# Optimization experiments

Measured on AMD Instinct MI355X. Metric: run time of the kernel, lower is better.

Reference implementation:

```python
import jax, jax.numpy as jnp
import numpy as np

B, L, D, H = 2, 2048, 2048, 16
DH = D // H

def setup_inputs() -> dict:
    key = jax.random.key(0)
    ks = jax.random.split(key, 7)
    q = jax.random.normal(ks[0], (B, L, D), dtype=jnp.float32)
    k = jax.random.normal(ks[1], (B, L, D), dtype=jnp.float32)
    v = jax.random.normal(ks[2], (B, L, D), dtype=jnp.float32)
    # causal mask: True means masked (matches torch masked_fill semantics)
    attn_mask = jnp.triu(jnp.ones((L, L), dtype=bool), k=1)[None, None, :, :]
    scale = 0.02
    wq = jax.random.normal(ks[3], (D, D), dtype=jnp.float32) * scale
    wk = jax.random.normal(ks[4], (D, D), dtype=jnp.float32) * scale
    wv = jax.random.normal(ks[5], (D, D), dtype=jnp.float32) * scale
    wo = jax.random.normal(ks[6], (D, D), dtype=jnp.float32) * scale
    return {"q": q, "k": k, "v": v, "attn_mask": attn_mask,
            "wq": wq, "wk": wk, "wv": wv, "wo": wo}

def _split_heads(x):
    b, l, _ = x.shape
    return x.reshape(b, l, H, DH).transpose(0, 2, 1, 3)  # [B,H,L,DH]

def reference(q, k, v, attn_mask, wq, wk, wv, wo):
    # torch Linear: y = x @ W.T (bias=False)
    qh = _split_heads(q @ wq.T)
    kh = _split_heads(k @ wk.T)
    vh = _split_heads(v @ wv.T)
    scale = 1.0 / np.sqrt(DH).astype(np.float32)
    scores = jnp.einsum('bhqd,bhkd->bhqk', qh, kh) * scale
    neg = jnp.finfo(scores.dtype).min
    scores = jnp.where(attn_mask, neg, scores)
    attn = jax.nn.softmax(scores, axis=-1)
    ctx = jnp.einsum('bhqk,bhkd->bhqd', attn, vh)
    ctx = ctx.transpose(0, 2, 1, 3).reshape(q.shape[0], q.shape[1], D)
    return ctx @ wo.T
```

## Files before the change

kernel.cpp:

```cpp
#include <hip/hip_runtime.h>

#define B_  2
#define L_  2048
#define D_  2048
#define H_  16
#define DH_ 128
#define K_  2048
#define M_  4096

typedef __attribute__((ext_vector_type(8))) short bf16x8;
typedef __attribute__((ext_vector_type(4))) float f32x4;
typedef __attribute__((ext_vector_type(4))) float float4v;
typedef __attribute__((ext_vector_type(8))) unsigned short u16x8;

__device__ __forceinline__ unsigned short f2bf(float f) {
  unsigned u = __builtin_bit_cast(unsigned, f);
  u += 0x7fffu + ((u >> 16) & 1u);
  return (unsigned short)(u >> 16);
}

typedef __attribute__((address_space(3))) unsigned int lds_uint;
typedef __attribute__((address_space(1))) const unsigned int glob_uint;
__device__ __forceinline__ void gld16(const void* g, void* l) {
  __builtin_amdgcn_global_load_lds((glob_uint*)g, (lds_uint*)l, 16, 0, 0);
}

__global__ void cvt_all(const float* __restrict__ wq, const float* __restrict__ wk,
                        const float* __restrict__ wv, const float* __restrict__ wo,
                        const float* __restrict__ q, const float* __restrict__ k,
                        const float* __restrict__ v, unsigned short* __restrict__ ws,
                        int nacts) {
  const size_t DD = (size_t)D_ * D_;
  const size_t BLD = (size_t)B_ * L_ * D_;
  const int z = blockIdx.z;
  const float* src;
  unsigned short* dst;
  size_t nelem;
  if (z < 4) {
    src = (z == 0) ? wq : (z == 1) ? wk : (z == 2) ? wv : wo;
    dst = ws + (size_t)z * DD;
    nelem = DD;
  } else {
    if (z - 4 >= nacts) return;
    src = (z == 4) ? q : (z == 5) ? k : v;
    dst = ws + 4 * DD + (size_t)(z - 4) * BLD;
    nelem = BLD;
  }
  size_t i = ((size_t)blockIdx.x * 256 + threadIdx.x) * 8;
  if (i >= nelem) return;
  float4v x0 = *(const float4v*)(src + i);
  float4v x1 = *(const float4v*)(src + i + 4);
  u16x8 p;
  p[0]=f2bf(x0[0]); p[1]=f2bf(x0[1]); p[2]=f2bf(x0[2]); p[3]=f2bf(x0[3]);
  p[4]=f2bf(x1[0]); p[5]=f2bf(x1[1]); p[6]=f2bf(x1[2]); p[7]=f2bf(x1[3]);
  *(u16x8*)(dst + i) = p;
}

template <bool ABF16>
__global__ __launch_bounds__(256, 2) void proj_gemm(
    const void* __restrict__ a0, const void* __restrict__ a1, const void* __restrict__ a2,
    const unsigned short* __restrict__ wqb, const unsigned short* __restrict__ wkb,
    const unsigned short* __restrict__ wvb,
    unsigned short* __restrict__ Qh, unsigned short* __restrict__ Kh,
    unsigned short* __restrict__ Vt) {
  __shared__ unsigned short smem[128 * 136];
  unsigned short* As = smem;
  unsigned short* Bs = smem + 128 * 64;

  const int z = blockIdx.z;
  const void* A = (z == 0) ? a0 : (z == 1) ? a1 : a2;
  const unsigned short* W = (z == 0) ? wqb : (z == 1) ? wkb : wvb;

  const int tid = threadIdx.x;
  const int wave = tid >> 6, lane = tid & 63;
  const int wr = wave >> 1, wc = wave & 1;
  const int bm0 = blockIdx.x * 128;
  const int bn0 = blockIdx.y * 128;
  const int l15 = lane & 15, l4 = lane >> 4;

  f32x4 acc[4][4];
#pragma unroll
  for (int m = 0; m < 4; m++)
#pragma unroll
    for (int n = 0; n < 4; n++) { f32x4 zz = {0.f, 0.f, 0.f, 0.f}; acc[m][n] = zz; }

  for (int k0 = 0; k0 < K_; k0 += 64) {
#pragma unroll
    for (int it = 0; it < 4; ++it) {
      const int base = it * 256 + wave * 64;
      const int ch = base + lane;
      const int r = ch >> 3, c = ch & 7;
      gld16(W + (size_t)(bn0 + r) * K_ + (k0 + c * 8), Bs + base * 8);
    }
    if (ABF16) {
#pragma unroll
      for (int it = 0; it < 4; ++it) {
        const int base = it * 256 + wave * 64;
        const int ch = base + lane;
        const int r = ch >> 3, c = ch & 7;
        gld16((const unsigned short*)A + (size_t)(bm0 + r) * K_ + (k0 + c * 8), As + base * 8);
      }
    } else {
#pragma unroll
      for (int it = 0; it < 4; ++it) {
        const int ch = it * 256 + tid;
        const int r = ch >> 3, c = ch & 7;
        const float* g = (const float*)A + (size_t)(bm0 + r) * K_ + (k0 + c * 8);
        float4v x0 = *(const float4v*)g;
        float4v x1 = *(const float4v*)(g + 4);
        u16x8 p;
        p[0]=f2bf(x0[0]); p[1]=f2bf(x0[1]); p[2]=f2bf(x0[2]); p[3]=f2bf(x0[3]);
        p[4]=f2bf(x1[0]); p[5]=f2bf(x1[1]); p[6]=f2bf(x1[2]); p[7]=f2bf(x1[3]);
        *(u16x8*)&As[ch * 8] = p;
      }
    }
    __syncthreads();
#pragma unroll
    for (int ks = 0; ks < 2; ++ks) {
      const int kc = ks * 32 + l4 * 8;
      bf16x8 af[4], bfr[4];
#pragma unroll
      for (int m = 0; m < 4; m++) af[m] = *(const bf16x8*)&As[(wr * 64 + m * 16 + l15) * 64 + kc];
#pragma unroll
      for (int n = 0; n < 4; n++) bfr[n] = *(const bf16x8*)&Bs[(wc * 64 + n * 16 + l15) * 64 + kc];
#pragma unroll
      for (int m = 0; m < 4; m++)
#pragma unroll
        for (int n = 0; n < 4; n++)
          acc[m][n] = __builtin_amdgcn_mfma_f32_16x16x32_bf16(af[m], bfr[n], acc[m][n], 0, 0, 0);
    }
    __syncthreads();
  }

  if (z < 2) {
    unsigned short* O = (z == 0) ? Qh : Kh;
#pragma unroll
    for (int m = 0; m < 4; m++) {
      const int rr = bm0 + wr * 64 + m * 16 + l4 * 4;
#pragma unroll
      for (int n = 0; n < 4; n++) {
        const int cc = bn0 + wc * 64 + n * 16 + l15;
        const int h = cc >> 7, dh = cc & 127;
#pragma unroll
        for (int j = 0; j < 4; j++) {
          const int r2 = rr + j;
          const int b = r2 >> 11, lr = r2 & 2047;
          O[((size_t)(b * H_ + h) * L_ + lr) * DH_ + dh] = f2bf(acc[m][n][j]);
        }
      }
    }
  } else {
    __syncthreads();
    unsigned short* T = smem;
#pragma unroll
    for (int m = 0; m < 4; m++)
#pragma unroll
      for (int n = 0; n < 4; n++) {
        const int cl = wc * 64 + n * 16 + l15;
        const int rl = wr * 64 + m * 16 + l4 * 4;
#pragma unroll
        for (int j = 0; j < 4; j++) T[cl * 136 + rl + j] = f2bf(acc[m][n][j]);
      }
    __syncthreads();
    const int b = bm0 >> 11, lbase = bm0 & 2047;
    const int hb = bn0 >> 7;
#pragma unroll
    for (int it = 0; it < 8; ++it) {
      const int idx = it * 256 + tid;
      const int dhl = idx >> 4, c = idx & 15;
      u16x8 val = *(const u16x8*)&T[dhl * 136 + c * 8];
      *(u16x8*)&Vt[((size_t)(b * H_ + hb) * DH_ + dhl) * L_ + lbase + c * 8] = val;
    }
  }
}

#define SCALE_ 0.08838834764831845f

__global__ __launch_bounds__(256, 2) void attn_kernel(
    const unsigned short* __restrict__ Qh, const unsigned short* __restrict__ Kh,
    const unsigned short* __restrict__ Vt, unsigned short* __restrict__ ctx) {
  __shared__ unsigned short Ks[128 * 128];
  __shared__ unsigned short Vs[128 * 128];
  __shared__ unsigned short Ps[4][16 * 128];

  const int pair = blockIdx.x, bh = blockIdx.y;
  const size_t hoff = (size_t)bh * L_ * DH_;
  const unsigned short* Qp = Qh + hoff;
  const unsigned short* Kp = Kh + hoff;
  const unsigned short* Vp = Vt + hoff;

  const int tid = threadIdx.x, wave = tid >> 6, lane = tid & 63;
  const int l15 = lane & 15, l4 = lane >> 4;
  const int b = bh >> 4, h = bh & 15;

#pragma unroll 1
  for (int p = 0; p < 2; ++p) {
    const int qt = p ? (31 - pair) : pair;
    const int ntiles = (qt + 2) >> 1;

    bf16x8 qf[4];
    {
      const int qrow = qt * 64 + wave * 16 + l15;
#pragma unroll
      for (int s = 0; s < 4; s++)
        qf[s] = *(const bf16x8*)&Qp[(size_t)qrow * DH_ + s * 32 + l4 * 8];
    }

    f32x4 o[8];
#pragma unroll
    for (int df = 0; df < 8; df++) { f32x4 zz = {0.f, 0.f, 0.f, 0.f}; o[df] = zz; }
    float m_r[4] = {-1e30f, -1e30f, -1e30f, -1e30f};
    float l_r[4] = {0.f, 0.f, 0.f, 0.f};

    for (int kt = 0; kt < ntiles; ++kt) {
#pragma unroll
      for (int it = 0; it < 8; ++it) {
        const int base = it * 256 + wave * 64;
        const int ch = base + lane;
        const int r = ch >> 4, s = ch & 15;
        gld16(Kp + (size_t)(kt * 128 + r) * DH_ + ((s ^ (r & 7)) * 8), (unsigned short*)Ks + base * 8);
      }
#pragma unroll
      for (int it = 0; it < 8; ++it) {
        const int base = it * 256 + wave * 64;
        const int ch = base + lane;
        const int r = ch >> 4, s = ch & 15;
        gld16(Vp + (size_t)r * L_ + kt * 128 + ((s ^ (r & 7)) * 8), (unsigned short*)Vs + base * 8);
      }
      __syncthreads();

      f32x4 sa[8];
#pragma unroll
      for (int f = 0; f < 8; f++) { f32x4 zz = {0.f, 0.f, 0.f, 0.f}; sa[f] = zz; }
#pragma unroll
      for (int ks = 0; ks < 4; ++ks) {
        const int c = ks * 4 + l4;
#pragma unroll
        for (int f = 0; f < 8; ++f) {
          const int n = f * 16 + l15;
          bf16x8 kf = *(const bf16x8*)&Ks[n * 128 + ((c ^ (n & 7)) * 8)];
          sa[f] = __builtin_amdgcn_mfma_f32_16x16x32_bf16(qf[ks], kf, sa[f], 0, 0, 0);
        }
      }

      const bool last = (kt == ntiles - 1);
#pragma unroll
      for (int f = 0; f < 8; f++) {
        const int kg = kt * 128 + f * 16 + l15;
#pragma unroll
        for (int j = 0; j < 4; j++) {
          float t = sa[f][j] * SCALE_;
          if (last && kg > qt * 64 + wave * 16 + l4 * 4 + j) t = -1e30f;
          sa[f][j] = t;
        }
      }

#pragma unroll
      for (int j = 0; j < 4; j++) {
        float mx = fmaxf(fmaxf(fmaxf(sa[0][j], sa[1][j]), fmaxf(sa[2][j], sa[3][j])),
                         fmaxf(fmaxf(sa[4][j], sa[5][j]), fmaxf(sa[6][j], sa[7][j])));
#pragma unroll
        for (int d = 1; d < 16; d <<= 1) mx = fmaxf(mx, __shfl_xor(mx, d));
        const float mnew = fmaxf(m_r[j], mx);
        const float alpha = __expf(m_r[j] - mnew);
        float rs = 0.f;
        const int row = l4 * 4 + j;
#pragma unroll
        for (int f = 0; f < 8; f++) {
          float pp = __expf(sa[f][j] - mnew);
          rs += pp;
          const int col = f * 16 + l15;
          const int c = col >> 3;
          Ps[wave][row * 128 + ((c ^ (row & 7)) * 8) + (col & 7)] = f2bf(pp);
        }
#pragma unroll
        for (int d = 1; d < 16; d <<= 1) rs += __shfl_xor(rs, d);
        l_r[j] = l_r[j] * alpha + rs;
        m_r[j] = mnew;
#pragma unroll
        for (int df = 0; df < 8; df++) o[df][j] *= alpha;
      }

#pragma unroll
      for (int ksl = 0; ksl < 4; ++ksl) {
        const int pc = ksl * 4 + l4;
        bf16x8 pf = *(const bf16x8*)&Ps[wave][l15 * 128 + ((pc ^ (l15 & 7)) * 8)];
#pragma unroll
        for (int df = 0; df < 8; ++df) {
          const int vr = df * 16 + l15;
          bf16x8 vf = *(const bf16x8*)&Vs[vr * 128 + ((pc ^ (vr & 7)) * 8)];
          o[df] = __builtin_amdgcn_mfma_f32_16x16x32_bf16(pf, vf, o[df], 0, 0, 0);
        }
      }
      __syncthreads();
    }

#pragma unroll
    for (int j = 0; j < 4; j++) {
      const float inv = 1.0f / l_r[j];
      const int lq = qt * 64 + wave * 16 + l4 * 4 + j;
      const size_t rowb = ((size_t)(b * L_ + lq)) * D_ + h * DH_;
#pragma unroll
      for (int df = 0; df < 8; ++df)
        ctx[rowb + df * 16 + l15] = f2bf(o[df][j] * inv);
    }
  }
}

__global__ __launch_bounds__(256, 2) void out_gemm(const unsigned short* __restrict__ ctx,
                                                   const unsigned short* __restrict__ wob,
                                                   float* __restrict__ out) {
  __shared__ unsigned short smem[2 * 128 * 64];
  unsigned short* As = smem;
  unsigned short* Bs = smem + 128 * 64;

  const int tid = threadIdx.x;
  const int wave = tid >> 6, lane = tid & 63;
  const int wr = wave >> 1, wc = wave & 1;
  const int bm0 = blockIdx.x * 128;
  const int bn0 = blockIdx.y * 128;
  const int l15 = lane & 15, l4 = lane >> 4;

  f32x4 acc[4][4];
#pragma unroll
  for (int m = 0; m < 4; m++)
#pragma unroll
    for (int n = 0; n < 4; n++) { f32x4 zz = {0.f, 0.f, 0.f, 0.f}; acc[m][n] = zz; }

  for (int k0 = 0; k0 < K_; k0 += 64) {
#pragma unroll
    for (int it = 0; it < 4; ++it) {
      const int base = it * 256 + wave * 64;
      const int ch = base + lane;
      const int r = ch >> 3, c = ch & 7;
      gld16(ctx + (size_t)(bm0 + r) * K_ + (k0 + c * 8), As + base * 8);
      gld16(wob + (size_t)(bn0 + r) * K_ + (k0 + c * 8), Bs + base * 8);
    }
    __syncthreads();
#pragma unroll
    for (int ks = 0; ks < 2; ++ks) {
      const int kc = ks * 32 + l4 * 8;
      bf16x8 af[4], bfr[4];
#pragma unroll
      for (int m = 0; m < 4; m++) af[m] = *(const bf16x8*)&As[(wr * 64 + m * 16 + l15) * 64 + kc];
#pragma unroll
      for (int n = 0; n < 4; n++) bfr[n] = *(const bf16x8*)&Bs[(wc * 64 + n * 16 + l15) * 64 + kc];
#pragma unroll
      for (int m = 0; m < 4; m++)
#pragma unroll
        for (int n = 0; n < 4; n++)
          acc[m][n] = __builtin_amdgcn_mfma_f32_16x16x32_bf16(af[m], bfr[n], acc[m][n], 0, 0, 0);
    }
    __syncthreads();
  }

#pragma unroll
  for (int m = 0; m < 4; m++) {
    const int rr = bm0 + wr * 64 + m * 16 + l4 * 4;
#pragma unroll
    for (int n = 0; n < 4; n++) {
      const int cc = bn0 + wc * 64 + n * 16 + l15;
#pragma unroll
      for (int j = 0; j < 4; j++) out[(size_t)(rr + j) * D_ + cc] = acc[m][n][j];
    }
  }
}

extern "C" void kernel_launch(void* const* d_in, const int* in_sizes, int n_in,
                              void* d_out, int out_size, void* d_ws, size_t ws_size,
                              hipStream_t stream) {
  const float* q  = (const float*)d_in[0];
  const float* k  = (const float*)d_in[1];
  const float* v  = (const float*)d_in[2];
  const float* wq = (const float*)d_in[4];
  const float* wk = (const float*)d_in[5];
  const float* wv = (const float*)d_in[6];
  const float* wo = (const float*)d_in[7];

  const size_t DD = (size_t)D_ * D_;
  const size_t BLD = (size_t)B_ * L_ * D_;
  unsigned short* ws  = (unsigned short*)d_ws;
  unsigned short* wqb = ws;
  unsigned short* wkb = wqb + DD;
  unsigned short* wvb = wkb + DD;
  unsigned short* wob = wvb + DD;

  const size_t need_full = (4 * DD + 7 * BLD) * 2;

  if (ws_size >= need_full) {
    unsigned short* qb  = wob + DD;
    unsigned short* kb  = qb + BLD;
    unsigned short* vb  = kb + BLD;
    unsigned short* QhP = vb + BLD;
    unsigned short* KhP = QhP + BLD;
    unsigned short* VtP = KhP + BLD;
    unsigned short* ctx = VtP + BLD;

    cvt_all<<<dim3(4096, 1, 7), 256, 0, stream>>>(wq, wk, wv, wo, q, k, v, ws, 3);
    proj_gemm<true><<<dim3(32, 16, 3), 256, 0, stream>>>(qb, kb, vb, wqb, wkb, wvb, QhP, KhP, VtP);
    attn_kernel<<<dim3(16, 32), 256, 0, stream>>>(QhP, KhP, VtP, ctx);
    out_gemm<<<dim3(32, 16), 256, 0, stream>>>(ctx, wob, (float*)d_out);
  } else {
    unsigned short* QhP = wob + DD;
    unsigned short* KhP = QhP + BLD;
    unsigned short* VtP = KhP + BLD;
    unsigned short* ctx = VtP + BLD;

    cvt_all<<<dim3(4096, 1, 4), 256, 0, stream>>>(wq, wk, wv, wo, q, k, v, ws, 0);
    proj_gemm<false><<<dim3(32, 16, 3), 256, 0, stream>>>(q, k, v, wqb, wkb, wvb, QhP, KhP, VtP);
    attn_kernel<<<dim3(16, 32), 256, 0, stream>>>(QhP, KhP, VtP, ctx);
    out_gemm<<<dim3(32, 16), 256, 0, stream>>>(ctx, wob, (float*)d_out);
  }
}
```

Measured before the change: 303.8 us.

## Replace projection and output GEMMs with triple-buffered 8-wave 128x256 GEMM

Adds a new gemm8 kernel with 512 threads and 128x256 tiles. It uses a three-stage LDS ring fed by direct global-to-LDS loads, XOR-swizzled LDS layouts, explicit vmcnt waits and barriers, s_setprio around MFMA bursts, and a block-index remap for L2 locality. It replaces both the QKV projection and the output projection, which previously used a single-buffered 128x128 GEMM that stalled on loads each k-step. The V transpose epilogue now uses vectorized swizzled LDS writes, and the attention kernel gets setprio hints around its MFMA loops. Costs are more LDS per block, which may lower occupancy, and more intricate synchronization.

```diff
diff --git a/kernel.cpp b/kernel.cpp
--- a/kernel.cpp
+++ b/kernel.cpp
@@ -6,12 +6,12 @@
 #define H_  16
 #define DH_ 128
 #define K_  2048
-#define M_  4096
 
 typedef __attribute__((ext_vector_type(8))) short bf16x8;
 typedef __attribute__((ext_vector_type(4))) float f32x4;
 typedef __attribute__((ext_vector_type(4))) float float4v;
 typedef __attribute__((ext_vector_type(8))) unsigned short u16x8;
+typedef __attribute__((ext_vector_type(4))) unsigned short u16x4;
 
 __device__ __forceinline__ unsigned short f2bf(float f) {
   unsigned u = __builtin_bit_cast(unsigned, f);
@@ -24,6 +24,9 @@
 __device__ __forceinline__ void gld16(const void* g, void* l) {
   __builtin_amdgcn_global_load_lds((glob_uint*)g, (lds_uint*)l, 16, 0, 0);
 }
+
+#define BAR() do { asm volatile("" ::: "memory"); __builtin_amdgcn_s_barrier(); asm volatile("" ::: "memory"); } while (0)
+#define VMCNT(n) asm volatile("s_waitcnt vmcnt(" #n ")" ::: "memory")
 
 __global__ void cvt_all(const float* __restrict__ wq, const float* __restrict__ wk,
                         const float* __restrict__ wv, const float* __restrict__ wo,
@@ -56,9 +59,192 @@
   *(u16x8*)(dst + i) = p;
 }
 
-template <bool ABF16>
-__global__ __launch_bounds__(256, 2) void proj_gemm(
-    const void* __restrict__ a0, const void* __restrict__ a1, const void* __restrict__ a2,
+template <int KIND>
+__global__ __launch_bounds__(512, 2) void gemm8(
+    const unsigned short* __restrict__ a0, const unsigned short* __restrict__ a1,
+    const unsigned short* __restrict__ a2,
+    const unsigned short* __restrict__ w0, const unsigned short* __restrict__ w1,
+    const unsigned short* __restrict__ w2,
+    unsigned short* __restrict__ Qh, unsigned short* __restrict__ Kh,
+    unsigned short* __restrict__ Vt, float* __restrict__ OF) {
+  __shared__ unsigned short smem[3 * 24576];
+
+  const int lin = blockIdx.x + 32 * (blockIdx.y + 8 * blockIdx.z);
+  const int cpx = KIND ? 32 : 96;
+  const int s = (lin & 7) * cpx + (lin >> 3);
+  const int mt = s & 31;
+  const int r_ = s >> 5;
+  const int ntile = KIND ? r_ : (r_ & 7);
+  const int z = KIND ? 0 : (r_ >> 3);
+
+  const unsigned short* A = KIND ? a0 : (z == 0 ? a0 : z == 1 ? a1 : a2);
+  const unsigned short* W = KIND ? w0 : (z == 0 ? w0 : z == 1 ? w1 : w2);
+  const int mode = KIND ? 2 : (z == 2 ? 1 : 0);
+
+  const int bm0 = mt * 128;
+  const int bn0 = ntile * 256;
+
+  const int tid = threadIdx.x;
+  const int wid = tid >> 6, lane = tid & 63;
+  const int wr = wid >> 2, wc = wid & 3;
+  const int l15 = lane & 15, l4 = lane >> 4;
+
+  const unsigned short* gsrc[6];
+  int ldst[6];
+  {
+#pragma unroll
+    for (int i = 0; i < 2; ++i) {
+      const int c = i * 512 + tid, r = c >> 3, s0 = c & 7;
+      gsrc[i] = A + (size_t)(bm0 + r) * K_ + ((s0 ^ (r & 7)) << 3);
+      ldst[i] = c * 8;
+    }
+#pragma unroll
+    for (int u = 0; u < 2; ++u)
+#pragma unroll
+      for (int i = 0; i < 2; ++i) {
+        const int c = i * 512 + tid, r = c >> 3, s0 = c & 7;
+        gsrc[2 + u * 2 + i] = W + (size_t)(bn0 + u * 128 + r) * K_ + ((s0 ^ (r & 7)) << 3);
+        ldst[2 + u * 2 + i] = 8192 + (u * 1024 + c) * 8;
+      }
+  }
+#define STAGE(idx, p) do { gld16(gsrc[idx], &smem[(p) * 24576 + ldst[idx]]); gsrc[idx] += 64; } while (0)
+
+  int offA[2][2][2], offB[4][2];
+#pragma unroll
+  for (int mh = 0; mh < 2; ++mh)
+#pragma unroll
+    for (int ml = 0; ml < 2; ++ml)
+#pragma unroll
+      for (int ks = 0; ks < 2; ++ks) {
+        const int row = wr * 64 + mh * 32 + ml * 16 + l15;
+        const int ch = ks * 4 + l4;
+        offA[mh][ml][ks] = row * 64 + ((ch ^ (row & 7)) << 3);
+      }
+#pragma unroll
+  for (int nf = 0; nf < 4; ++nf)
+#pragma unroll
+    for (int ks = 0; ks < 2; ++ks) {
+      const int rowb = wc * 64 + nf * 16 + l15;
+      const int ch = ks * 4 + l4;
+      offB[nf][ks] = 8192 + rowb * 64 + ((ch ^ (rowb & 7)) << 3);
+    }
+
+  f32x4 acc[4][4];
+#pragma unroll
+  for (int m = 0; m < 4; ++m)
+#pragma unroll
+    for (int n = 0; n < 4; ++n) { f32x4 zz = {0.f, 0.f, 0.f, 0.f}; acc[m][n] = zz; }
+
+  STAGE(0, 0); STAGE(1, 0); STAGE(2, 0); STAGE(3, 0); STAGE(4, 0); STAGE(5, 0);
+  STAGE(0, 1); STAGE(1, 1); STAGE(2, 1); STAGE(3, 1); STAGE(4, 1); STAGE(5, 1);
+  VMCNT(6);
+  BAR();
+
+  int p = 0;
+  for (int t = 0; t < 32; ++t) {
+    int p2 = p + 2; if (p2 >= 3) p2 -= 3;
+    const unsigned short* bA = &smem[p * 24576];
+    bf16x8 af[2][2], bfr[4][2];
+#pragma unroll
+    for (int ml = 0; ml < 2; ++ml)
+#pragma unroll
+      for (int ks = 0; ks < 2; ++ks)
+        af[ml][ks] = *(const bf16x8*)&bA[offA[0][ml][ks]];
+#pragma unroll
+    for (int nf = 0; nf < 4; ++nf)
+#pragma unroll
+      for (int ks = 0; ks < 2; ++ks)
+        bfr[nf][ks] = *(const bf16x8*)&bA[offB[nf][ks]];
+    if (t < 30) { STAGE(0, p2); STAGE(1, p2); STAGE(2, p2); STAGE(3, p2); }
+    BAR();
+    __builtin_amdgcn_s_setprio(1);
+#pragma unroll
+    for (int ml = 0; ml < 2; ++ml)
+#pragma unroll
+      for (int nf = 0; nf < 4; ++nf)
+#pragma unroll
+        for (int ks = 0; ks < 2; ++ks)
+          acc[ml][nf] = __builtin_amdgcn_mfma_f32_16x16x32_bf16(af[ml][ks], bfr[nf][ks], acc[ml][nf], 0, 0, 0);
+    __builtin_amdgcn_s_setprio(0);
+    BAR();
+#pragma unroll
+    for (int ml = 0; ml < 2; ++ml)
+#pragma unroll
+      for (int ks = 0; ks < 2; ++ks)
+        af[ml][ks] = *(const bf16x8*)&bA[offA[1][ml][ks]];
+    if (t < 30) { STAGE(4, p2); STAGE(5, p2); }
+    BAR();
+    __builtin_amdgcn_s_setprio(1);
+#pragma unroll
+    for (int ml = 0; ml < 2; ++ml)
+#pragma unroll
+      for (int nf = 0; nf < 4; ++nf)
+#pragma unroll
+        for (int ks = 0; ks < 2; ++ks)
+          acc[2 + ml][nf] = __builtin_amdgcn_mfma_f32_16x16x32_bf16(af[ml][ks], bfr[nf][ks], acc[2 + ml][nf], 0, 0, 0);
+    __builtin_amdgcn_s_setprio(0);
+    if (t < 30) { VMCNT(6); } else { VMCNT(0); }
+    BAR();
+    p = (p == 2) ? 0 : p + 1;
+  }
+#undef STAGE
+
+  if (mode == 0) {
+    unsigned short* O = (z == 0) ? Qh : Kh;
+#pragma unroll
+    for (int mf = 0; mf < 4; ++mf) {
+      const int rr = bm0 + wr * 64 + mf * 16 + l4 * 4;
+#pragma unroll
+      for (int nf = 0; nf < 4; ++nf) {
+        const int cc = bn0 + wc * 64 + nf * 16 + l15;
+        const int h = cc >> 7, dh = cc & 127;
+#pragma unroll
+        for (int j = 0; j < 4; ++j) {
+          const int r2 = rr + j;
+          O[((size_t)((r2 >> 11) * H_ + h) * L_ + (r2 & 2047)) * DH_ + dh] = f2bf(acc[mf][nf][j]);
+        }
+      }
+    }
+  } else if (mode == 1) {
+    unsigned short* T = smem;
+#pragma unroll
+    for (int mf = 0; mf < 4; ++mf) {
+      const int rl = wr * 64 + mf * 16 + l4 * 4;
+#pragma unroll
+      for (int nf = 0; nf < 4; ++nf) {
+        const int cl = wc * 64 + nf * 16 + l15;
+        u16x4 vv;
+#pragma unroll
+        for (int j = 0; j < 4; ++j) vv[j] = f2bf(acc[mf][nf][j]);
+        *(u16x4*)&T[cl * 128 + (((rl >> 3) ^ (cl & 7)) << 3) + (rl & 7)] = vv;
+      }
+    }
+    __syncthreads();
+    const int b = bm0 >> 11, lbase = bm0 & 2047;
+#pragma unroll
+    for (int it = 0; it < 8; ++it) {
+      const int idx = it * 512 + tid;
+      const int rT = idx >> 4, sT = idx & 15;
+      u16x8 val = *(const u16x8*)&T[rT * 128 + ((sT ^ (rT & 7)) << 3)];
+      const int n = bn0 + rT, h = n >> 7, dh = n & 127;
+      *(u16x8*)&Vt[((size_t)(b * H_ + h) * DH_ + dh) * L_ + lbase + sT * 8] = val;
+    }
+  } else {
+#pragma unroll
+    for (int mf = 0; mf < 4; ++mf) {
+      const int rr = bm0 + wr * 64 + mf * 16 + l4 * 4;
+#pragma unroll
+      for (int nf = 0; nf < 4; ++nf) {
+        const int cc = bn0 + wc * 64 + nf * 16 + l15;
+#pragma unroll
+        for (int j = 0; j < 4; ++j) OF[(size_t)(rr + j) * D_ + cc] = acc[mf][nf][j];
+      }
+    }
+  }
+}
+
+__global__ __launch_bounds__(256, 2) void proj_gemm_f32a(
+    const float* __restrict__ q, const float* __restrict__ k, const float* __restrict__ v,
     const unsigned short* __restrict__ wqb, const unsigned short* __restrict__ wkb,
     const unsigned short* __restrict__ wvb,
     unsigned short* __restrict__ Qh, unsigned short* __restrict__ Kh,
@@ -68,7 +254,7 @@
   unsigned short* Bs = smem + 128 * 64;
 
   const int z = blockIdx.z;
-  const void* A = (z == 0) ? a0 : (z == 1) ? a1 : a2;
+  const float* A = (z == 0) ? q : (z == 1) ? k : v;
   const unsigned short* W = (z == 0) ? wqb : (z == 1) ? wkb : wvb;
 
   const int tid = threadIdx.x;
@@ -92,27 +278,17 @@
       const int r = ch >> 3, c = ch & 7;
       gld16(W + (size_t)(bn0 + r) * K_ + (k0 + c * 8), Bs + base * 8);
     }
-    if (ABF16) {
-#pragma unroll
-      for (int it = 0; it < 4; ++it) {
-        const int base = it * 256 + wave * 64;
-        const int ch = base + lane;
-        const int r = ch >> 3, c = ch & 7;
-        gld16((const unsigned short*)A + (size_t)(bm0 + r) * K_ + (k0 + c * 8), As + base * 8);
-      }
-    } else {
-#pragma unroll
-      for (int it = 0; it < 4; ++it) {
-        const int ch = it * 256 + tid;
-        const int r = ch >> 3, c = ch & 7;
-        const float* g = (const float*)A + (size_t)(bm0 + r) * K_ + (k0 + c * 8);
-        float4v x0 = *(const float4v*)g;
-        float4v x1 = *(const float4v*)(g + 4);
-        u16x8 p;
-        p[0]=f2bf(x0[0]); p[1]=f2bf(x0[1]); p[2]=f2bf(x0[2]); p[3]=f2bf(x0[3]);
-        p[4]=f2bf(x1[0]); p[5]=f2bf(x1[1]); p[6]=f2bf(x1[2]); p[7]=f2bf(x1[3]);
-        *(u16x8*)&As[ch * 8] = p;
-      }
+#pragma unroll
+    for (int it = 0; it < 4; ++it) {
+      const int ch = it * 256 + tid;
+      const int r = ch >> 3, c = ch & 7;
+      const float* g = A + (size_t)(bm0 + r) * K_ + (k0 + c * 8);
+      float4v x0 = *(const float4v*)g;
+      float4v x1 = *(const float4v*)(g + 4);
+      u16x8 pp;
+      pp[0]=f2bf(x0[0]); pp[1]=f2bf(x0[1]); pp[2]=f2bf(x0[2]); pp[3]=f2bf(x0[3]);
+      pp[4]=f2bf(x1[0]); pp[5]=f2bf(x1[1]); pp[6]=f2bf(x1[2]); pp[7]=f2bf(x1[3]);
+      *(u16x8*)&As[ch * 8] = pp;
     }
     __syncthreads();
 #pragma unroll
@@ -144,8 +320,7 @@
 #pragma unroll
         for (int j = 0; j < 4; j++) {
           const int r2 = rr + j;
-          const int b = r2 >> 11, lr = r2 & 2047;
-          O[((size_t)(b * H_ + h) * L_ + lr) * DH_ + dh] = f2bf(acc[m][n][j]);
+          O[((size_t)((r2 >> 11) * H_ + h) * L_ + (r2 & 2047)) * DH_ + dh] = f2bf(acc[m][n][j]);
         }
       }
     }
@@ -232,6 +407,7 @@
       f32x4 sa[8];
 #pragma unroll
       for (int f = 0; f < 8; f++) { f32x4 zz = {0.f, 0.f, 0.f, 0.f}; sa[f] = zz; }
+      __builtin_amdgcn_s_setprio(1);
 #pragma unroll
       for (int ks = 0; ks < 4; ++ks) {
         const int c = ks * 4 + l4;
@@ -242,6 +418,7 @@
           sa[f] = __builtin_amdgcn_mfma_f32_16x16x32_bf16(qf[ks], kf, sa[f], 0, 0, 0);
         }
       }
+      __builtin_amdgcn_s_setprio(0);
 
       const bool last = (kt == ntiles - 1);
 #pragma unroll
@@ -281,6 +458,7 @@
         for (int df = 0; df < 8; df++) o[df][j] *= alpha;
       }
 
+      __builtin_amdgcn_s_setprio(1);
 #pragma unroll
       for (int ksl = 0; ksl < 4; ++ksl) {
         const int pc = ksl * 4 + l4;
@@ -292,6 +470,7 @@
           o[df] = __builtin_amdgcn_mfma_f32_16x16x32_bf16(pf, vf, o[df], 0, 0, 0);
         }
       }
+      __builtin_amdgcn_s_setprio(0);
       __syncthreads();
     }
 
@@ -303,65 +482,6 @@
 #pragma unroll
       for (int df = 0; df < 8; ++df)
         ctx[rowb + df * 16 + l15] = f2bf(o[df][j] * inv);
-    }
-  }
-}
-
-__global__ __launch_bounds__(256, 2) void out_gemm(const unsigned short* __restrict__ ctx,
-                                                   const unsigned short* __restrict__ wob,
-                                                   float* __restrict__ out) {
-  __shared__ unsigned short smem[2 * 128 * 64];
-  unsigned short* As = smem;
-  unsigned short* Bs = smem + 128 * 64;
-
-  const int tid = threadIdx.x;
-  const int wave = tid >> 6, lane = tid & 63;
-  const int wr = wave >> 1, wc = wave & 1;
-  const int bm0 = blockIdx.x * 128;
-  const int bn0 = blockIdx.y * 128;
-  const int l15 = lane & 15, l4 = lane >> 4;
-
-  f32x4 acc[4][4];
-#pragma unroll
-  for (int m = 0; m < 4; m++)
-#pragma unroll
-    for (int n = 0; n < 4; n++) { f32x4 zz = {0.f, 0.f, 0.f, 0.f}; acc[m][n] = zz; }
-
-  for (int k0 = 0; k0 < K_; k0 += 64) {
-#pragma unroll
-    for (int it = 0; it < 4; ++it) {
-      const int base = it * 256 + wave * 64;
-      const int ch = base + lane;
-      const int r = ch >> 3, c = ch & 7;
-      gld16(ctx + (size_t)(bm0 + r) * K_ + (k0 + c * 8), As + base * 8);
-      gld16(wob + (size_t)(bn0 + r) * K_ + (k0 + c * 8), Bs + base * 8);
-    }
-    __syncthreads();
-#pragma unroll
-    for (int ks = 0; ks < 2; ++ks) {
-      const int kc = ks * 32 + l4 * 8;
-      bf16x8 af[4], bfr[4];
-#pragma unroll
-      for (int m = 0; m < 4; m++) af[m] = *(const bf16x8*)&As[(wr * 64 + m * 16 + l15) * 64 + kc];
-#pragma unroll
-      for (int n = 0; n < 4; n++) bfr[n] = *(const bf16x8*)&Bs[(wc * 64 + n * 16 + l15) * 64 + kc];
-#pragma unroll
-      for (int m = 0; m < 4; m++)
-#pragma unroll
-        for (int n = 0; n < 4; n++)
-          acc[m][n] = __builtin_amdgcn_mfma_f32_16x16x32_bf16(af[m], bfr[n], acc[m][n], 0, 0, 0);
-    }
-    __syncthreads();
-  }
-
-#pragma unroll
-  for (int m = 0; m < 4; m++) {
-    const int rr = bm0 + wr * 64 + m * 16 + l4 * 4;
-#pragma unroll
-    for (int n = 0; n < 4; n++) {
-      const int cc = bn0 + wc * 64 + n * 16 + l15;
-#pragma unroll
-      for (int j = 0; j < 4; j++) out[(size_t)(rr + j) * D_ + cc] = acc[m][n][j];
     }
   }
 }
@@ -397,9 +517,10 @@
     unsigned short* ctx = VtP + BLD;
 
     cvt_all<<<dim3(4096, 1, 7), 256, 0, stream>>>(wq, wk, wv, wo, q, k, v, ws, 3);
-    proj_gemm<true><<<dim3(32, 16, 3), 256, 0, stream>>>(qb, kb, vb, wqb, wkb, wvb, QhP, KhP, VtP);
+    gemm8<0><<<dim3(32, 8, 3), 512, 0, stream>>>(qb, kb, vb, wqb, wkb, wvb, QhP, KhP, VtP, nullptr);
     attn_kernel<<<dim3(16, 32), 256, 0, stream>>>(QhP, KhP, VtP, ctx);
-    out_gemm<<<dim3(32, 16), 256, 0, stream>>>(ctx, wob, (float*)d_out);
+    gemm8<1><<<dim3(32, 8, 1), 512, 0, stream>>>(ctx, nullptr, nullptr, wob, nullptr, nullptr,
+                                                 nullptr, nullptr, nullptr, (float*)d_out);
   } else {
     unsigned short* QhP = wob + DD;
     unsigned short* KhP = QhP + BLD;
@@ -407,8 +528,9 @@
     unsigned short* ctx = VtP + BLD;
 
     cvt_all<<<dim3(4096, 1, 4), 256, 0, stream>>>(wq, wk, wv, wo, q, k, v, ws, 0);
-    proj_gemm<false><<<dim3(32, 16, 3), 256, 0, stream>>>(q, k, v, wqb, wkb, wvb, QhP, KhP, VtP);
+    proj_gemm_f32a<<<dim3(32, 16, 3), 256, 0, stream>>>(q, k, v, wqb, wkb, wvb, QhP, KhP, VtP);
     attn_kernel<<<dim3(16, 32), 256, 0, stream>>>(QhP, KhP, VtP, ctx);
-    out_gemm<<<dim3(32, 16), 256, 0, stream>>>(ctx, wob, (float*)d_out);
-  }
-}
+    gemm8<1><<<dim3(32, 8, 1), 512, 0, stream>>>(ctx, nullptr, nullptr, wob, nullptr, nullptr,
+                                                 nullptr, nullptr, nullptr, (float*)d_out);
+  }
+}
```

Measured after the change: 291.3 us. -4.1%, faster.
